# Kernel optimization log

Hardware: AMD Instinct MI355X
Metric: run time of the kernel (lower is better)

Reference implementation:

```python
import jax, jax.numpy as jnp
import numpy as np

C = 64


def setup_inputs() -> dict:
    key = jax.random.key(0)
    ks = jax.random.split(key, 7)
    x = jax.random.normal(ks[0], (8, C, 64, 64), dtype=jnp.float32)
    # 1x1 conv weights stored as [out_c, in_c]; biases [out_c]
    s = 1.0 / np.sqrt(C)
    W1 = jax.random.uniform(ks[1], (C, C), jnp.float32, -s, s)
    b1 = jax.random.uniform(ks[2], (C,), jnp.float32, -s, s)
    W2 = jax.random.uniform(ks[3], (C, C), jnp.float32, -s, s)
    b2 = jax.random.uniform(ks[4], (C,), jnp.float32, -s, s)
    W3 = jax.random.uniform(ks[5], (C, C), jnp.float32, -s, s)
    b3 = jax.random.uniform(ks[6], (C,), jnp.float32, -s, s)
    return {"x": x, "W1": W1, "b1": b1, "W2": W2, "b2": b2, "W3": W3, "b3": b3}


def reference(x, W1, b1, W2, b2, W3, b3):
    gamma = 1.0
    b, c, h, w = x.shape
    xf = x.reshape(b, c, h * w)  # [b, c, n]
    # 1x1 convs == per-pixel channel matmuls
    f = jnp.einsum('oc,bcn->bon', W1, xf) + b1[None, :, None]
    g = jnp.einsum('oc,bcn->bon', W2, xf) + b2[None, :, None]
    k = jnp.einsum('oc,bcn->bon', W3, xf) + b3[None, :, None]
    # scores[b,i,j] = sum_c f[b,c,i] * g[b,c,j]; softmax over j
    scores = jnp.einsum('bci,bcj->bij', f, g)
    attn = jax.nn.softmax(scores, axis=2)
    # out_attn[b,c,i] = sum_j attn[b,i,j] * k[b,c,j]
    out = jnp.einsum('bij,bcj->bci', attn, k).reshape(b, c, h, w)
    return gamma * out + x
```

## Files before the change

kernel.cpp:

```cpp
#include <hip/hip_runtime.h>
#include <hip/hip_bf16.h>

#define NPIX 4096
#define CCH  64
#define NB   8
#define KVBLK 64

typedef __attribute__((ext_vector_type(8)))  short short8;
typedef __attribute__((ext_vector_type(4)))  float f32x4;
typedef __attribute__((ext_vector_type(16))) float f32x16;

#define LOG2E   1.44269504f

__global__ __launch_bounds__(256) void proj_kernel(
    const float* __restrict__ x,
    const float* __restrict__ W1, const float* __restrict__ b1,
    const float* __restrict__ W2, const float* __restrict__ b2,
    const float* __restrict__ W3, const float* __restrict__ b3,
    __hip_bfloat16* __restrict__ Q, __hip_bfloat16* __restrict__ G,
    __hip_bfloat16* __restrict__ K)
{
    const int m    = blockIdx.x % 3;
    const int tile = blockIdx.x / 3;
    const int b    = tile >> 6;
    const int i0   = (tile & 63) << 6;

    const float* W  = (m == 0) ? W1 : (m == 1) ? W2 : W3;
    const float* bv = (m == 0) ? b1 : (m == 1) ? b2 : b3;

    __shared__ float xs[64][65];
    __shared__ float Wt[64][68];

    for (int e = threadIdx.x; e < 4096; e += 256) {
        const int c = e >> 6, p = e & 63;
        xs[c][p] = x[(size_t)b * CCH * NPIX + (size_t)c * NPIX + i0 + p];
        Wt[e & 63][e >> 6] = W[e];
    }
    __syncthreads();

    const int p = threadIdx.x & 63;
    const int g = threadIdx.x >> 6;

    float acc[16];
    #pragma unroll
    for (int oo = 0; oo < 16; ++oo) acc[oo] = bv[g * 16 + oo];

    for (int c = 0; c < 64; ++c) {
        const float xv = xs[c][p];
        const f32x4* w = (const f32x4*)&Wt[c][g * 16];
        #pragma unroll
        for (int qq = 0; qq < 4; ++qq) {
            const f32x4 a = w[qq];
            #pragma unroll
            for (int j = 0; j < 4; ++j)
                acc[qq * 4 + j] += a[j] * xv;
        }
    }

    const int i = i0 + p;
    if (m == 0) {
        #pragma unroll
        for (int oo = 0; oo < 16; ++oo)
            Q[(size_t)b * NPIX * CCH + (size_t)i * CCH + g * 16 + oo] =
                __float2bfloat16(acc[oo] * LOG2E);
    } else if (m == 1) {
        #pragma unroll
        for (int oo = 0; oo < 16; ++oo)
            G[(size_t)b * NPIX * CCH + (size_t)i * CCH + g * 16 + oo] =
                __float2bfloat16(acc[oo]);
    } else {
        #pragma unroll
        for (int oo = 0; oo < 16; ++oo)
            K[(size_t)b * CCH * NPIX + (size_t)(g * 16 + oo) * NPIX + i] =
                __float2bfloat16(acc[oo]);
    }
}

__device__ __forceinline__ void gload_lds16(const void* g, void* l) {
    __builtin_amdgcn_global_load_lds(
        (const __attribute__((address_space(1))) unsigned int*)g,
        (__attribute__((address_space(3))) unsigned int*)l, 16, 0, 0);
}
__device__ __forceinline__ unsigned int pack_bf16(float lo, float hi) {
    union { __hip_bfloat162 h; unsigned int u; } w;
    w.h = __float22bfloat162_rn(make_float2(lo, hi));
    return w.u;
}
__device__ __forceinline__ void pipe_barrier() {
    asm volatile("s_waitcnt vmcnt(2)" ::: "memory");
    __builtin_amdgcn_sched_barrier(0);
    __builtin_amdgcn_s_barrier();
    __builtin_amdgcn_sched_barrier(0);
}

__global__ __launch_bounds__(512, 4) void attn_kernel(
    const __hip_bfloat16* __restrict__ Qg, const __hip_bfloat16* __restrict__ Gg,
    const __hip_bfloat16* __restrict__ Kg,
    __hip_bfloat16* __restrict__ Opart, float* __restrict__ Lpart, int split)
{
    __shared__ char lds[3][16384];

    const int blk   = blockIdx.x;
    const int per_b = 16 * split;
    const int b     = blk / per_b;
    const int rem   = blk - b * per_b;
    const int itile = rem / split;
    const int sp    = rem - itile * split;
    const int tid   = threadIdx.x;
    const int wave  = tid >> 6;
    const int lane  = tid & 63;
    const int l32   = lane & 31;
    const int hi    = lane >> 5;
    const int i0w   = itile * 256 + wave * 32;
    const int jcnt  = NPIX / split;
    const int jlo   = sp * jcnt;
    const int niter = jcnt / KVBLK;

    const short* Qb = (const short*)Qg + (size_t)b * NPIX * CCH;
    const char*  Gb = (const char*)(Gg + (size_t)b * NPIX * CCH);
    const char*  Kb = (const char*)(Kg + (size_t)b * CCH * NPIX);

    short8 q[4];
    #pragma unroll
    for (int ks = 0; ks < 4; ++ks)
        q[ks] = *(const short8*)(Qb + (size_t)(i0w + l32) * CCH + ks * 16 + hi * 8);

    int gbase[2], kbase[2];
    #pragma unroll
    for (int jb = 0; jb < 2; ++jb)
        gbase[jb] = (jb * 32 + l32) * 128 + ((l32 & 7) << 4);
    #pragma unroll
    for (int cb = 0; cb < 2; ++cb)
        kbase[cb] = 8192 + (cb * 32 + l32) * 128 + ((l32 & 7) << 4);

    const int srow = tid >> 3, scolb = (tid & 7) * 16;
    const char* gsrc = Gb + (size_t)(jlo + srow) * 128 + (scolb ^ ((srow & 7) << 4));
    const char* ksrc = Kb + (size_t)srow * 8192 + (size_t)jlo * 2 + (scolb ^ ((srow & 7) << 4));

    f32x16 zacc;
    #pragma unroll
    for (int r = 0; r < 16; ++r) zacc[r] = 0.f;

    f32x16 o[2];
    #pragma unroll
    for (int cb = 0; cb < 2; ++cb)
        #pragma unroll
        for (int r = 0; r < 16; ++r) o[cb][r] = 0.f;
    float ps = 0.f;

    auto STAGE = [&](int buf, int tt) {
        gload_lds16(gsrc + tt * (KVBLK * 128), lds[buf] + wave * 1024);
        gload_lds16(ksrc + tt * (KVBLK * 2),  lds[buf] + 8192 + wave * 1024);
    };

    STAGE(0, 0);
    STAGE(1, 1);
    pipe_barrier();

    int cur = 0;
    for (int t = 0; t < niter; ++t) {
        const int nxt2 = (cur == 0) ? 2 : (cur == 1) ? 0 : 1;
        STAGE(nxt2, (t + 2 < niter) ? t + 2 : 0);
        const char* L = lds[cur];

        #pragma unroll
        for (int jb = 0; jb < 2; ++jb) {
            short8 ga[4];
            #pragma unroll
            for (int ks = 0; ks < 4; ++ks)
                ga[ks] = *(const short8*)(L + (gbase[jb] ^ ((2 * ks + hi) << 4)));

            __builtin_amdgcn_s_setprio(1);
            f32x16 acc = __builtin_amdgcn_mfma_f32_32x32x16_bf16(ga[0], q[0], zacc, 0, 0, 0);
            acc = __builtin_amdgcn_mfma_f32_32x32x16_bf16(ga[1], q[1], acc, 0, 0, 0);
            acc = __builtin_amdgcn_mfma_f32_32x32x16_bf16(ga[2], q[2], acc, 0, 0, 0);
            acc = __builtin_amdgcn_mfma_f32_32x32x16_bf16(ga[3], q[3], acc, 0, 0, 0);
            __builtin_amdgcn_s_setprio(0);

            float p[16];
            #pragma unroll
            for (int r = 0; r < 16; ++r) {
                p[r] = __builtin_amdgcn_exp2f(acc[r]);
                ps += p[r];
            }
            short8 pf[2];
            #pragma unroll
            for (int kk = 0; kk < 2; ++kk) {
                unsigned int x0 = pack_bf16(p[8 * kk + 0], p[8 * kk + 1]);
                unsigned int x1 = pack_bf16(p[8 * kk + 2], p[8 * kk + 3]);
                unsigned int y0 = pack_bf16(p[8 * kk + 4], p[8 * kk + 5]);
                unsigned int y1 = pack_bf16(p[8 * kk + 6], p[8 * kk + 7]);
                asm("v_permlane32_swap_b32 %0, %1" : "+v"(x0), "+v"(y0));
                asm("v_permlane32_swap_b32 %0, %1" : "+v"(x1), "+v"(y1));
                union { unsigned int u[4]; short8 v; } w;
                w.u[0] = x0; w.u[1] = x1; w.u[2] = y0; w.u[3] = y1;
                pf[kk] = w.v;
            }

            __builtin_amdgcn_s_setprio(1);
            #pragma unroll
            for (int kk = 0; kk < 2; ++kk) {
                const int ksg = 2 * jb + kk;
                const short8 ka0 = *(const short8*)(L + (kbase[0] ^ ((2 * ksg + hi) << 4)));
                const short8 ka1 = *(const short8*)(L + (kbase[1] ^ ((2 * ksg + hi) << 4)));
                o[0] = __builtin_amdgcn_mfma_f32_32x32x16_bf16(ka0, pf[kk], o[0], 0, 0, 0);
                o[1] = __builtin_amdgcn_mfma_f32_32x32x16_bf16(ka1, pf[kk], o[1], 0, 0, 0);
            }
            __builtin_amdgcn_s_setprio(0);
        }
        pipe_barrier();
        cur = (cur == 2) ? 0 : cur + 1;
    }

    const size_t pb = (size_t)(b * split + sp);
    #pragma unroll
    for (int cb = 0; cb < 2; ++cb)
        #pragma unroll
        for (int r = 0; r < 16; ++r) {
            const int c = cb * 32 + (r & 3) + 8 * (r >> 2) + 4 * hi;
            const int i = i0w + l32;
            Opart[(pb * CCH + c) * NPIX + i] = __float2bfloat16(o[cb][r]);
        }
    ps += __shfl_xor(ps, 32);
    if (lane < 32)
        Lpart[pb * NPIX + i0w + l32] = ps;
}

__global__ __launch_bounds__(256) void combine_kernel(
    const __hip_bfloat16* __restrict__ Opart, const float* __restrict__ Lpart,
    const float* __restrict__ x, float* __restrict__ out, int split)
{
    const int b  = blockIdx.x >> 6;
    const int i0 = (blockIdx.x & 63) << 6;

    __shared__ float invL[64];
    if (threadIdx.x < 64) {
        const int i = i0 + threadIdx.x;
        float L = 0.f;
        for (int s = 0; s < split; ++s)
            L += Lpart[((size_t)(b * split + s)) * NPIX + i];
        invL[threadIdx.x] = 1.0f / L;
    }
    __syncthreads();

    const int c    = threadIdx.x >> 2;
    const int ioff = (threadIdx.x & 3) * 16;

    float acc[16];
    #pragma unroll
    for (int k = 0; k < 16; ++k) acc[k] = 0.f;

    for (int s = 0; s < split; ++s) {
        const size_t base = (((size_t)(b * split + s)) * CCH + c) * NPIX + i0 + ioff;
        const short8 v0 = *(const short8*)((const short*)Opart + base);
        const short8 v1 = *(const short8*)((const short*)Opart + base + 8);
        #pragma unroll
        for (int k = 0; k < 8; ++k) {
            union { unsigned int u; float f; } cv0, cv1;
            cv0.u = ((unsigned int)(unsigned short)v0[k]) << 16;
            cv1.u = ((unsigned int)(unsigned short)v1[k]) << 16;
            acc[k]     += cv0.f;
            acc[k + 8] += cv1.f;
        }
    }

    const size_t idx = ((size_t)b * CCH + c) * NPIX + i0 + ioff;
    #pragma unroll
    for (int kq = 0; kq < 4; ++kq) {
        const f32x4 xv = *(const f32x4*)&x[idx + 4 * kq];
        f32x4 r;
        #pragma unroll
        for (int t = 0; t < 4; ++t)
            r[t] = acc[kq * 4 + t] * invL[ioff + kq * 4 + t] + xv[t];
        *(f32x4*)&out[idx + 4 * kq] = r;
    }
}

extern "C" void kernel_launch(void* const* d_in, const int* in_sizes, int n_in,
                              void* d_out, int out_size, void* d_ws, size_t ws_size,
                              hipStream_t stream) {
    const float* x  = (const float*)d_in[0];
    const float* W1 = (const float*)d_in[1];
    const float* b1 = (const float*)d_in[2];
    const float* W2 = (const float*)d_in[3];
    const float* b2 = (const float*)d_in[4];
    const float* W3 = (const float*)d_in[5];
    const float* b3 = (const float*)d_in[6];
    float* out = (float*)d_out;

    char* ws = (char*)d_ws;
    const size_t planeB = (size_t)NB * NPIX * CCH * sizeof(__hip_bfloat16);
    __hip_bfloat16* Q = (__hip_bfloat16*)(ws);
    __hip_bfloat16* G = (__hip_bfloat16*)(ws + planeB);
    __hip_bfloat16* K = (__hip_bfloat16*)(ws + 2 * planeB);

    const size_t base   = 3 * planeB;
    const size_t oPlane = planeB;
    const size_t lPlane = (size_t)NB * NPIX * sizeof(float);

    int split = 8;
    while (split > 1 && base + (size_t)split * (oPlane + lPlane) > ws_size)
        split >>= 1;

    __hip_bfloat16* Opart = (__hip_bfloat16*)(ws + base);
    float* Lpart = (float*)(ws + base + (size_t)split * oPlane);

    proj_kernel<<<dim3(NB * 64 * 3), dim3(256), 0, stream>>>(x, W1, b1, W2, b2, W3, b3, Q, G, K);
    attn_kernel<<<dim3(NB * 16 * split), dim3(512), 0, stream>>>(Q, G, K, Opart, Lpart, split);
    combine_kernel<<<dim3(NB * 64), dim3(256), 0, stream>>>(Opart, Lpart, x, out, split);
}
```

Before: 83.32 us.

## Process two query tiles per wave with 256-thread blocks and double buffering

The attention kernel now uses 4 waves of 256 threads, each handling 64 query rows (two 32-row MFMA tiles), so every G/K fragment read from LDS is reused across two query tiles. The triple-buffered pipeline with a partial vmcnt wait becomes a double buffer synchronised with __syncthreads, and each thread now issues two async loads per operand. The aim is to halve LDS traffic per MFMA and cut barrier participants. In exchange it raises register pressure from doubled accumulators and weakens load/compute overlap because the full barrier waits for all outstanding loads.

```diff
diff --git a/kernel.cpp b/kernel.cpp
--- a/kernel.cpp
+++ b/kernel.cpp
@@ -86,19 +86,13 @@
     w.h = __float22bfloat162_rn(make_float2(lo, hi));
     return w.u;
 }
-__device__ __forceinline__ void pipe_barrier() {
-    asm volatile("s_waitcnt vmcnt(2)" ::: "memory");
-    __builtin_amdgcn_sched_barrier(0);
-    __builtin_amdgcn_s_barrier();
-    __builtin_amdgcn_sched_barrier(0);
-}
-
-__global__ __launch_bounds__(512, 4) void attn_kernel(
+
+__global__ __launch_bounds__(256, 4) void attn_kernel(
     const __hip_bfloat16* __restrict__ Qg, const __hip_bfloat16* __restrict__ Gg,
     const __hip_bfloat16* __restrict__ Kg,
     __hip_bfloat16* __restrict__ Opart, float* __restrict__ Lpart, int split)
 {
-    __shared__ char lds[3][16384];
+    __shared__ char lds[2][16384];
 
     const int blk   = blockIdx.x;
     const int per_b = 16 * split;
@@ -111,7 +105,7 @@
     const int lane  = tid & 63;
     const int l32   = lane & 31;
     const int hi    = lane >> 5;
-    const int i0w   = itile * 256 + wave * 32;
+    const int i0w   = itile * 256 + wave * 64;
     const int jcnt  = NPIX / split;
     const int jlo   = sp * jcnt;
     const int niter = jcnt / KVBLK;
@@ -120,10 +114,12 @@
     const char*  Gb = (const char*)(Gg + (size_t)b * NPIX * CCH);
     const char*  Kb = (const char*)(Kg + (size_t)b * CCH * NPIX);
 
-    short8 q[4];
-    #pragma unroll
-    for (int ks = 0; ks < 4; ++ks)
-        q[ks] = *(const short8*)(Qb + (size_t)(i0w + l32) * CCH + ks * 16 + hi * 8);
+    short8 q[2][4];
+    #pragma unroll
+    for (int ib = 0; ib < 2; ++ib)
+        #pragma unroll
+        for (int ks = 0; ks < 4; ++ks)
+            q[ib][ks] = *(const short8*)(Qb + (size_t)(i0w + ib * 32 + l32) * CCH + ks * 16 + hi * 8);
 
     int gbase[2], kbase[2];
     #pragma unroll
@@ -133,34 +129,43 @@
     for (int cb = 0; cb < 2; ++cb)
         kbase[cb] = 8192 + (cb * 32 + l32) * 128 + ((l32 & 7) << 4);
 
-    const int srow = tid >> 3, scolb = (tid & 7) * 16;
-    const char* gsrc = Gb + (size_t)(jlo + srow) * 128 + (scolb ^ ((srow & 7) << 4));
-    const char* ksrc = Kb + (size_t)srow * 8192 + (size_t)jlo * 2 + (scolb ^ ((srow & 7) << 4));
+    const char* gsrc[2]; const char* ksrc[2];
+    #pragma unroll
+    for (int r = 0; r < 2; ++r) {
+        const int off = r * 4096 + wave * 1024 + lane * 16;
+        const int row = off >> 7, colb = off & 127;
+        gsrc[r] = Gb + (size_t)(jlo + row) * 128 + (colb ^ ((row & 7) << 4));
+        ksrc[r] = Kb + (size_t)row * 8192 + (size_t)jlo * 2 + (colb ^ ((row & 7) << 4));
+    }
 
     f32x16 zacc;
     #pragma unroll
     for (int r = 0; r < 16; ++r) zacc[r] = 0.f;
 
-    f32x16 o[2];
-    #pragma unroll
-    for (int cb = 0; cb < 2; ++cb)
-        #pragma unroll
-        for (int r = 0; r < 16; ++r) o[cb][r] = 0.f;
-    float ps = 0.f;
+    f32x16 o[2][2];
+    #pragma unroll
+    for (int ib = 0; ib < 2; ++ib)
+        #pragma unroll
+        for (int cb = 0; cb < 2; ++cb)
+            #pragma unroll
+            for (int r = 0; r < 16; ++r) o[ib][cb][r] = 0.f;
+    float ps[2] = {0.f, 0.f};
 
     auto STAGE = [&](int buf, int tt) {
-        gload_lds16(gsrc + tt * (KVBLK * 128), lds[buf] + wave * 1024);
-        gload_lds16(ksrc + tt * (KVBLK * 2),  lds[buf] + 8192 + wave * 1024);
+        #pragma unroll
+        for (int r = 0; r < 2; ++r)
+            gload_lds16(gsrc[r] + tt * (KVBLK * 128), lds[buf] + r * 4096 + wave * 1024);
+        #pragma unroll
+        for (int r = 0; r < 2; ++r)
+            gload_lds16(ksrc[r] + tt * (KVBLK * 2), lds[buf] + 8192 + r * 4096 + wave * 1024);
     };
 
     STAGE(0, 0);
-    STAGE(1, 1);
-    pipe_barrier();
-
-    int cur = 0;
+    __syncthreads();
+
     for (int t = 0; t < niter; ++t) {
-        const int nxt2 = (cur == 0) ? 2 : (cur == 1) ? 0 : 1;
-        STAGE(nxt2, (t + 2 < niter) ? t + 2 : 0);
+        const int cur = t & 1;
+        STAGE(cur ^ 1, (t + 1 < niter) ? t + 1 : 0);
         const char* L = lds[cur];
 
         #pragma unroll
@@ -170,31 +175,34 @@
             for (int ks = 0; ks < 4; ++ks)
                 ga[ks] = *(const short8*)(L + (gbase[jb] ^ ((2 * ks + hi) << 4)));
 
-            __builtin_amdgcn_s_setprio(1);
-            f32x16 acc = __builtin_amdgcn_mfma_f32_32x32x16_bf16(ga[0], q[0], zacc, 0, 0, 0);
-            acc = __builtin_amdgcn_mfma_f32_32x32x16_bf16(ga[1], q[1], acc, 0, 0, 0);
-            acc = __builtin_amdgcn_mfma_f32_32x32x16_bf16(ga[2], q[2], acc, 0, 0, 0);
-            acc = __builtin_amdgcn_mfma_f32_32x32x16_bf16(ga[3], q[3], acc, 0, 0, 0);
-            __builtin_amdgcn_s_setprio(0);
-
-            float p[16];
-            #pragma unroll
-            for (int r = 0; r < 16; ++r) {
-                p[r] = __builtin_amdgcn_exp2f(acc[r]);
-                ps += p[r];
-            }
-            short8 pf[2];
-            #pragma unroll
-            for (int kk = 0; kk < 2; ++kk) {
-                unsigned int x0 = pack_bf16(p[8 * kk + 0], p[8 * kk + 1]);
-                unsigned int x1 = pack_bf16(p[8 * kk + 2], p[8 * kk + 3]);
-                unsigned int y0 = pack_bf16(p[8 * kk + 4], p[8 * kk + 5]);
-                unsigned int y1 = pack_bf16(p[8 * kk + 6], p[8 * kk + 7]);
-                asm("v_permlane32_swap_b32 %0, %1" : "+v"(x0), "+v"(y0));
-                asm("v_permlane32_swap_b32 %0, %1" : "+v"(x1), "+v"(y1));
-                union { unsigned int u[4]; short8 v; } w;
-                w.u[0] = x0; w.u[1] = x1; w.u[2] = y0; w.u[3] = y1;
-                pf[kk] = w.v;
+            short8 pf[2][2];
+            #pragma unroll
+            for (int ib = 0; ib < 2; ++ib) {
+                __builtin_amdgcn_s_setprio(1);
+                f32x16 acc = __builtin_amdgcn_mfma_f32_32x32x16_bf16(ga[0], q[ib][0], zacc, 0, 0, 0);
+                acc = __builtin_amdgcn_mfma_f32_32x32x16_bf16(ga[1], q[ib][1], acc, 0, 0, 0);
+                acc = __builtin_amdgcn_mfma_f32_32x32x16_bf16(ga[2], q[ib][2], acc, 0, 0, 0);
+                acc = __builtin_amdgcn_mfma_f32_32x32x16_bf16(ga[3], q[ib][3], acc, 0, 0, 0);
+                __builtin_amdgcn_s_setprio(0);
+
+                float p[16];
+                #pragma unroll
+                for (int r = 0; r < 16; ++r) {
+                    p[r] = __builtin_amdgcn_exp2f(acc[r]);
+                    ps[ib] += p[r];
+                }
+                #pragma unroll
+                for (int kk = 0; kk < 2; ++kk) {
+                    unsigned int x0 = pack_bf16(p[8 * kk + 0], p[8 * kk + 1]);
+                    unsigned int x1 = pack_bf16(p[8 * kk + 2], p[8 * kk + 3]);
+                    unsigned int y0 = pack_bf16(p[8 * kk + 4], p[8 * kk + 5]);
+                    unsigned int y1 = pack_bf16(p[8 * kk + 6], p[8 * kk + 7]);
+                    asm("v_permlane32_swap_b32 %0, %1" : "+v"(x0), "+v"(y0));
+                    asm("v_permlane32_swap_b32 %0, %1" : "+v"(x1), "+v"(y1));
+                    union { unsigned int u[4]; short8 v; } w;
+                    w.u[0] = x0; w.u[1] = x1; w.u[2] = y0; w.u[3] = y1;
+                    pf[ib][kk] = w.v;
+                }
             }
 
             __builtin_amdgcn_s_setprio(1);
@@ -203,27 +211,32 @@
                 const int ksg = 2 * jb + kk;
                 const short8 ka0 = *(const short8*)(L + (kbase[0] ^ ((2 * ksg + hi) << 4)));
                 const short8 ka1 = *(const short8*)(L + (kbase[1] ^ ((2 * ksg + hi) << 4)));
-                o[0] = __builtin_amdgcn_mfma_f32_32x32x16_bf16(ka0, pf[kk], o[0], 0, 0, 0);
-                o[1] = __builtin_amdgcn_mfma_f32_32x32x16_bf16(ka1, pf[kk], o[1], 0, 0, 0);
+                #pragma unroll
+                for (int ib = 0; ib < 2; ++ib) {
+                    o[ib][0] = __builtin_amdgcn_mfma_f32_32x32x16_bf16(ka0, pf[ib][kk], o[ib][0], 0, 0, 0);
+                    o[ib][1] = __builtin_amdgcn_mfma_f32_32x32x16_bf16(ka1, pf[ib][kk], o[ib][1], 0, 0, 0);
+                }
             }
             __builtin_amdgcn_s_setprio(0);
         }
-        pipe_barrier();
-        cur = (cur == 2) ? 0 : cur + 1;
+        __syncthreads();
     }
 
     const size_t pb = (size_t)(b * split + sp);
     #pragma unroll
-    for (int cb = 0; cb < 2; ++cb)
-        #pragma unroll
-        for (int r = 0; r < 16; ++r) {
-            const int c = cb * 32 + (r & 3) + 8 * (r >> 2) + 4 * hi;
-            const int i = i0w + l32;
-            Opart[(pb * CCH + c) * NPIX + i] = __float2bfloat16(o[cb][r]);
-        }
-    ps += __shfl_xor(ps, 32);
-    if (lane < 32)
-        Lpart[pb * NPIX + i0w + l32] = ps;
+    for (int ib = 0; ib < 2; ++ib) {
+        #pragma unroll
+        for (int cb = 0; cb < 2; ++cb)
+            #pragma unroll
+            for (int r = 0; r < 16; ++r) {
+                const int c = cb * 32 + (r & 3) + 8 * (r >> 2) + 4 * hi;
+                const int i = i0w + ib * 32 + l32;
+                Opart[(pb * CCH + c) * NPIX + i] = __float2bfloat16(o[ib][cb][r]);
+            }
+        ps[ib] += __shfl_xor(ps[ib], 32);
+        if (lane < 32)
+            Lpart[pb * NPIX + i0w + ib * 32 + l32] = ps[ib];
+    }
 }
 
 __global__ __launch_bounds__(256) void combine_kernel(
@@ -306,6 +319,6 @@
     float* Lpart = (float*)(ws + base + (size_t)split * oPlane);
 
     proj_kernel<<<dim3(NB * 64 * 3), dim3(256), 0, stream>>>(x, W1, b1, W2, b2, W3, b3, Q, G, K);
-    attn_kernel<<<dim3(NB * 16 * split), dim3(512), 0, stream>>>(Q, G, K, Opart, Lpart, split);
+    attn_kernel<<<dim3(NB * 16 * split), dim3(256), 0, stream>>>(Q, G, K, Opart, Lpart, split);
     combine_kernel<<<dim3(NB * 64), dim3(256), 0, stream>>>(Opart, Lpart, x, out, split);
 }
```

After: 265.3 us. +218.4%, slower.
